# Kernel optimization log

Hardware: AMD Instinct MI355X
Metric: run time of the kernel (lower is better)

The kernel has to match this reference:

```python
import jax, jax.numpy as jnp
import numpy as np
from math import sqrt

N_IN = 1024
N_OUT = 1024
DEPTH = 10
N_NODES = 2 ** (DEPTH + 1) - 1  # 2047
BATCH = 32768


def setup_inputs() -> dict:
    key = jax.random.key(0)
    k1, k2, k3 = jax.random.split(key, 3)
    f1 = 1.0 / sqrt(N_IN)
    f2 = 1.0 / sqrt(DEPTH + 1)
    x = jax.random.normal(k1, (BATCH, N_IN), dtype=jnp.float32)
    w1s = jax.random.uniform(k2, (N_NODES, N_IN), dtype=jnp.float32, minval=-f1, maxval=f1)
    w2s = jax.random.uniform(k3, (N_NODES, N_OUT), dtype=jnp.float32, minval=-f2, maxval=f2)
    return {"x": x, "w1s": w1s, "w2s": w2s, "depth": DEPTH}


def reference(x, w1s, w2s, depth):
    batch = x.shape[0]

    def step(current_node, _):
        # current_node: [b] int32 node index at this tree level
        plane_score = jnp.einsum('bi,bi->b', x, w1s[current_node])  # [b]
        plane_choice = (plane_score > 0).astype(jnp.int32)
        next_node = current_node * 2 + plane_choice + 1
        return next_node, (current_node, plane_score)

    node0 = jnp.zeros((batch,), dtype=jnp.int32)
    _, (all_nodes, all_scores) = jax.lax.scan(step, node0, None, length=depth + 1)
    all_nodes = all_nodes.T    # [b, depth+1]
    all_scores = all_scores.T  # [b, depth+1]

    selected_w2s = w2s[all_nodes]  # [b, depth+1, nOut]
    y = jnp.einsum('bij,bi->bj', selected_w2s, all_scores)
    return y
```

## Files before the change

kernel.cpp:

```cpp
#include <hip/hip_runtime.h>


typedef float        f32x4 __attribute__((ext_vector_type(4)));
typedef unsigned int u32x4 __attribute__((ext_vector_type(4)));

#define FFF_BATCH  32768
#define FFF_NIN    1024
#define FFF_NOUT   1024
#define FFF_LEVELS 11
#define FFF_NODES  2047
#define FFF_EPS    0.035f

__device__ __forceinline__ f32x4 ld_nt4f(const f32x4* p) { return __builtin_nontemporal_load(p); }
__device__ __forceinline__ float ub(unsigned d, int k) {
    return (float)((d >> (8 * k)) & 0xffu);
}

__device__ __forceinline__ int sdot4(unsigned a, unsigned b, int c) {
#if __has_builtin(__builtin_amdgcn_sdot4)
    return __builtin_amdgcn_sdot4((int)a, (int)b, c, false);
#else
#pragma unroll
    for (int k = 0; k < 4; ++k) {
        const int ai = (int)(a << (24 - 8 * k)) >> 24;
        const int bi = (int)(b << (24 - 8 * k)) >> 24;
        c += ai * bi;
    }
    return c;
#endif
}

template<int CTRL>
__device__ __forceinline__ float dpp_add(float v) {
    const int t = __builtin_amdgcn_update_dpp(0, __float_as_int(v), CTRL, 0xF, 0xF, true);
    return v + __int_as_float(t);
}
__device__ __forceinline__ float wave_sum(float v) {
    v = dpp_add<0x111>(v); v = dpp_add<0x112>(v);
    v = dpp_add<0x114>(v); v = dpp_add<0x118>(v);
    v = dpp_add<0x142>(v); v = dpp_add<0x143>(v);
    return __int_as_float(__builtin_amdgcn_readlane(__float_as_int(v), 63));
}
template<int CTRL>
__device__ __forceinline__ int dpp_addi(int v) {
    return v + __builtin_amdgcn_update_dpp(0, v, CTRL, 0xF, 0xF, true);
}
__device__ __forceinline__ int wave_sum_i(int v) {
    v = dpp_addi<0x111>(v); v = dpp_addi<0x112>(v);
    v = dpp_addi<0x114>(v); v = dpp_addi<0x118>(v);
    v = dpp_addi<0x142>(v); v = dpp_addi<0x143>(v);
    return __builtin_amdgcn_readlane(v, 63);
}
template<int CTRL>
__device__ __forceinline__ float dpp_max(float v) {
    const int t = __builtin_amdgcn_update_dpp(0, __float_as_int(v), CTRL, 0xF, 0xF, true);
    return fmaxf(v, __int_as_float(t));
}
__device__ __forceinline__ float wave_max(float v) {
    v = dpp_max<0x111>(v); v = dpp_max<0x112>(v);
    v = dpp_max<0x114>(v); v = dpp_max<0x118>(v);
    v = dpp_max<0x142>(v); v = dpp_max<0x143>(v);
    return __int_as_float(__builtin_amdgcn_readlane(__float_as_int(v), 63));
}

__global__ void fff_quant_u8(const float* __restrict__ w1, const float* __restrict__ w2,
                             unsigned char* __restrict__ q1, unsigned char* __restrict__ q2,
                             float* __restrict__ s1, float* __restrict__ s2)
{
    const int node = blockIdx.x;
    const int t    = threadIdx.x;
    const int wave = t >> 6;
    const int lane = t & 63;

    const f32x4* r1 = reinterpret_cast<const f32x4*>(w1 + (size_t)node * FFF_NIN);
    const f32x4* r2 = reinterpret_cast<const f32x4*>(w2 + (size_t)node * FFF_NOUT);
    const int si = 64 * (t & 3) + (t >> 2);
    const f32x4 v1 = r1[si];
    const f32x4 v2 = r2[si];

    float m1 = 0.f, m2 = 0.f;
#pragma unroll
    for (int k = 0; k < 4; ++k) {
        m1 = fmaxf(m1, fabsf(v1[k]));
        m2 = fmaxf(m2, fabsf(v2[k]));
    }
#pragma unroll
    for (int m = 1; m < 64; m <<= 1) {
        m1 = fmaxf(m1, __shfl_xor(m1, m, 64));
        m2 = fmaxf(m2, __shfl_xor(m2, m, 64));
    }
    __shared__ float sm1[4], sm2[4];
    if (lane == 0) { sm1[wave] = m1; sm2[wave] = m2; }
    __syncthreads();
    m1 = fmaxf(fmaxf(sm1[0], sm1[1]), fmaxf(sm1[2], sm1[3]));
    m2 = fmaxf(fmaxf(sm2[0], sm2[1]), fmaxf(sm2[2], sm2[3]));

    const float st1 = (m1 > 0.f) ? m1 / 127.f : 1.f;
    const float st2 = (m2 > 0.f) ? m2 / 127.f : 1.f;
    if (t == 0) { s1[node] = st1; s2[node] = st2; }

    unsigned d1 = 0, d2 = 0;
#pragma unroll
    for (int k = 0; k < 4; ++k) {
        const int i1 = (int)rintf(v1[k] / st1);
        const int u2 = (int)rintf(v2[k] / st2) + 128;
        d1 |= ((unsigned)i1 & 0xffu) << (8 * k);
        d2 |= ((unsigned)u2 & 0xffu) << (8 * k);
    }
    reinterpret_cast<unsigned*>(q1)[(size_t)node * 256 + t] = d1;
    reinterpret_cast<unsigned*>(q2)[(size_t)node * 256 + t] = d2;
}

__global__ __launch_bounds__(256, 4) void fff_main_u8(
    const float*         __restrict__ x,
    const unsigned char* __restrict__ q1,
    const float*         __restrict__ s1,
    const float*         __restrict__ w1f,
    const unsigned char* __restrict__ q2,
    const float*         __restrict__ s2,
    float*               __restrict__ y)
{
    const int row  = blockIdx.x * 4 + (threadIdx.x >> 6);
    const int lane = threadIdx.x & 63;

    const f32x4* x4 = reinterpret_cast<const f32x4*>(x + (size_t)row * FFF_NIN);
    f32x4 xv[4];
#pragma unroll
    for (int c = 0; c < 4; ++c) xv[c] = ld_nt4f(&x4[c * 64 + lane]);

    float mx = 0.f;
#pragma unroll
    for (int c = 0; c < 4; ++c)
#pragma unroll
        for (int k = 0; k < 4; ++k) mx = fmaxf(mx, fabsf(xv[c][k]));
    mx = wave_max(mx);
    const float stx = (mx > 0.f) ? mx / 127.f : 1.f;
    const float inv = (mx > 0.f) ? 127.f / mx : 0.f;

    unsigned xq[4];
#pragma unroll
    for (int c = 0; c < 4; ++c) {
        const int a0 = (int)rintf(xv[c][0] * inv);
        const int a1 = (int)rintf(xv[c][1] * inv);
        const int a2 = (int)rintf(xv[c][2] * inv);
        const int a3 = (int)rintf(xv[c][3] * inv);
        xq[c] = ((unsigned)a0 & 0xffu) | (((unsigned)a1 & 0xffu) << 8) |
                (((unsigned)a2 & 0xffu) << 16) | (((unsigned)a3 & 0xffu) << 24);
    }

    f32x4 acc[4];
#pragma unroll
    for (int c = 0; c < 4; ++c) acc[c] = (f32x4)(0.f);
    float corr = 0.f;

    const u32x4* q1v = reinterpret_cast<const u32x4*>(q1);
    const u32x4* q2v = reinterpret_cast<const u32x4*>(q2);

    int node = 0;
    u32x4 d1 = q1v[lane];
    u32x4 d2 = q2v[lane];
    float sc1 = s1[0];
    float sc2 = s2[0];

#pragma unroll 1
    for (int l = 0; l < FFF_LEVELS; ++l) {
        int idot = 0;
#pragma unroll
        for (int c = 0; c < 4; ++c) idot = sdot4(xq[c], d1[c], idot);

        float p = (float)wave_sum_i(idot) * (stx * sc1);

        if (__builtin_expect(fabsf(p) < FFF_EPS, 0)) {
            const f32x4* w14 = reinterpret_cast<const f32x4*>(w1f + (size_t)node * FFF_NIN);
            float s = 0.f;
#pragma unroll
            for (int c = 0; c < 4; ++c) {
                const f32x4 w = w14[c * 64 + lane];
                s = fmaf(xv[c][0], w[0], s);
                s = fmaf(xv[c][1], w[1], s);
                s = fmaf(xv[c][2], w[2], s);
                s = fmaf(xv[c][3], w[3], s);
            }
            p = wave_sum(s);
        }

        const int next = 2 * node + 1 + ((p > 0.f) ? 1 : 0);
        u32x4 nd1 = d1, nd2 = d2;
        float ns1 = sc1, ns2 = sc2;
        if (l < FFF_LEVELS - 1) {
            const int un = __builtin_amdgcn_readfirstlane(next);
            nd1 = q1v[(size_t)un * 64 + lane];
            nd2 = q2v[(size_t)un * 64 + lane];
            ns1 = s1[un];
            ns2 = s2[un];
        }

        const float s2l = p * sc2;
        corr = fmaf(s2l, 128.f, corr);
#pragma unroll
        for (int c = 0; c < 4; ++c) {
#pragma unroll
            for (int k = 0; k < 4; ++k)
                acc[c][k] = fmaf(s2l, ub(d2[c], k), acc[c][k]);
        }

        node = next;
        d1 = nd1; d2 = nd2; sc1 = ns1; sc2 = ns2;
    }

    f32x4* y4 = reinterpret_cast<f32x4*>(y + (size_t)row * FFF_NOUT);
#pragma unroll
    for (int c = 0; c < 4; ++c) {
        f32x4 o;
        o[0] = acc[c][0] - corr; o[1] = acc[c][1] - corr;
        o[2] = acc[c][2] - corr; o[3] = acc[c][3] - corr;
        y4[c * 64 + lane] = o;
    }
}

__global__ __launch_bounds__(256, 4) void fff_fused_f32(
    const float* __restrict__ x, const float* __restrict__ w1s,
    const float* __restrict__ w2s, float* __restrict__ y)
{
    const int row  = blockIdx.x * 4 + (threadIdx.x >> 6);
    const int lane = threadIdx.x & 63;
    const f32x4* x4 = reinterpret_cast<const f32x4*>(x + (size_t)row * FFF_NIN);
    f32x4 xv[4];
#pragma unroll
    for (int c = 0; c < 4; ++c) xv[c] = x4[c * 64 + lane];
    f32x4 acc[4];
#pragma unroll
    for (int c = 0; c < 4; ++c) acc[c] = (f32x4)(0.f);
    int node = 0;
#pragma unroll 1
    for (int l = 0; l < FFF_LEVELS; ++l) {
        const f32x4* w14 = reinterpret_cast<const f32x4*>(w1s + (size_t)node * FFF_NIN);
        const f32x4* w24 = reinterpret_cast<const f32x4*>(w2s + (size_t)node * FFF_NOUT);
        f32x4 wv[4], uv[4];
#pragma unroll
        for (int c = 0; c < 4; ++c) { wv[c] = w14[c * 64 + lane]; uv[c] = w24[c * 64 + lane]; }
        float p = 0.f;
#pragma unroll
        for (int c = 0; c < 4; ++c) {
            p = fmaf(xv[c][0], wv[c][0], p); p = fmaf(xv[c][1], wv[c][1], p);
            p = fmaf(xv[c][2], wv[c][2], p); p = fmaf(xv[c][3], wv[c][3], p);
        }
#pragma unroll
        for (int m = 1; m < 64; m <<= 1) p += __shfl_xor(p, m, 64);
#pragma unroll
        for (int c = 0; c < 4; ++c) {
            acc[c][0] = fmaf(p, uv[c][0], acc[c][0]); acc[c][1] = fmaf(p, uv[c][1], acc[c][1]);
            acc[c][2] = fmaf(p, uv[c][2], acc[c][2]); acc[c][3] = fmaf(p, uv[c][3], acc[c][3]);
        }
        node = node * 2 + 1 + ((p > 0.f) ? 1 : 0);
    }
    f32x4* y4 = reinterpret_cast<f32x4*>(y + (size_t)row * FFF_NOUT);
#pragma unroll
    for (int c = 0; c < 4; ++c) y4[c * 64 + lane] = acc[c];
}

extern "C" void kernel_launch(void* const* d_in, const int* in_sizes, int n_in,
                              void* d_out, int out_size, void* d_ws, size_t ws_size,
                              hipStream_t stream) {
    const float* x   = (const float*)d_in[0];
    const float* w1s = (const float*)d_in[1];
    const float* w2s = (const float*)d_in[2];
    float* y = (float*)d_out;

    const size_t sc_bytes = 8192;
    const size_t q_bytes  = (size_t)FFF_NODES * 1024;
    const size_t need = 2 * sc_bytes + 2 * q_bytes;

    if (ws_size >= need) {
        float* s1 = (float*)d_ws;
        float* s2 = (float*)((char*)d_ws + sc_bytes);
        unsigned char* q1 = (unsigned char*)d_ws + 2 * sc_bytes;
        unsigned char* q2 = q1 + q_bytes;
        fff_quant_u8<<<FFF_NODES, 256, 0, stream>>>(w1s, w2s, q1, q2, s1, s2);
        fff_main_u8<<<FFF_BATCH / 4, 256, 0, stream>>>(x, q1, s1, w1s, q2, s2, y);
    } else {
        fff_fused_f32<<<FFF_BATCH / 4, 256, 0, stream>>>(x, w1s, w2s, y);
    }
}
```

Measured before the change: 80.45 us.

## Process two batch rows per wavefront with interleaved tree traversal

Each wavefront now handles two batch rows, interleaving their int8 dot products, paired DPP reductions and next-node weight loads, so the two independent dependency chains can hide each other's latency. The fp32 row data is no longer kept in registers; the rare exact-recheck path reloads x from memory instead. The grid is halved to match. This raises register pressure and may lower occupancy, and both rows' fallback branches can diverge in cost.

```diff
diff --git a/kernel.cpp b/kernel.cpp
--- a/kernel.cpp
+++ b/kernel.cpp
@@ -45,11 +45,15 @@
 __device__ __forceinline__ int dpp_addi(int v) {
     return v + __builtin_amdgcn_update_dpp(0, v, CTRL, 0xF, 0xF, true);
 }
-__device__ __forceinline__ int wave_sum_i(int v) {
-    v = dpp_addi<0x111>(v); v = dpp_addi<0x112>(v);
-    v = dpp_addi<0x114>(v); v = dpp_addi<0x118>(v);
-    v = dpp_addi<0x142>(v); v = dpp_addi<0x143>(v);
-    return __builtin_amdgcn_readlane(v, 63);
+__device__ __forceinline__ void wave_sum_i2(int& a, int& b) {
+    a = dpp_addi<0x111>(a); b = dpp_addi<0x111>(b);
+    a = dpp_addi<0x112>(a); b = dpp_addi<0x112>(b);
+    a = dpp_addi<0x114>(a); b = dpp_addi<0x114>(b);
+    a = dpp_addi<0x118>(a); b = dpp_addi<0x118>(b);
+    a = dpp_addi<0x142>(a); b = dpp_addi<0x142>(b);
+    a = dpp_addi<0x143>(a); b = dpp_addi<0x143>(b);
+    a = __builtin_amdgcn_readlane(a, 63);
+    b = __builtin_amdgcn_readlane(b, 63);
 }
 template<int CTRL>
 __device__ __forceinline__ float dpp_max(float v) {
@@ -120,101 +124,145 @@
     const float*         __restrict__ s2,
     float*               __restrict__ y)
 {
-    const int row  = blockIdx.x * 4 + (threadIdx.x >> 6);
+    const int wave = threadIdx.x >> 6;
     const int lane = threadIdx.x & 63;
-
-    const f32x4* x4 = reinterpret_cast<const f32x4*>(x + (size_t)row * FFF_NIN);
-    f32x4 xv[4];
-#pragma unroll
-    for (int c = 0; c < 4; ++c) xv[c] = ld_nt4f(&x4[c * 64 + lane]);
-
-    float mx = 0.f;
-#pragma unroll
-    for (int c = 0; c < 4; ++c)
-#pragma unroll
-        for (int k = 0; k < 4; ++k) mx = fmaxf(mx, fabsf(xv[c][k]));
-    mx = wave_max(mx);
-    const float stx = (mx > 0.f) ? mx / 127.f : 1.f;
-    const float inv = (mx > 0.f) ? 127.f / mx : 0.f;
-
-    unsigned xq[4];
-#pragma unroll
-    for (int c = 0; c < 4; ++c) {
-        const int a0 = (int)rintf(xv[c][0] * inv);
-        const int a1 = (int)rintf(xv[c][1] * inv);
-        const int a2 = (int)rintf(xv[c][2] * inv);
-        const int a3 = (int)rintf(xv[c][3] * inv);
-        xq[c] = ((unsigned)a0 & 0xffu) | (((unsigned)a1 & 0xffu) << 8) |
-                (((unsigned)a2 & 0xffu) << 16) | (((unsigned)a3 & 0xffu) << 24);
-    }
-
-    f32x4 acc[4];
-#pragma unroll
-    for (int c = 0; c < 4; ++c) acc[c] = (f32x4)(0.f);
-    float corr = 0.f;
+    const int row0 = (blockIdx.x * 4 + wave) * 2;
+
+    const f32x4* x4a = reinterpret_cast<const f32x4*>(x + (size_t)row0 * FFF_NIN);
+    const f32x4* x4b = reinterpret_cast<const f32x4*>(x + (size_t)(row0 + 1) * FFF_NIN);
+
+    unsigned xqa[4], xqb[4];
+    float stxa, stxb;
+    {
+        f32x4 xa[4], xb[4];
+#pragma unroll
+        for (int c = 0; c < 4; ++c) {
+            xa[c] = ld_nt4f(&x4a[c * 64 + lane]);
+            xb[c] = ld_nt4f(&x4b[c * 64 + lane]);
+        }
+        float ma = 0.f, mb = 0.f;
+#pragma unroll
+        for (int c = 0; c < 4; ++c)
+#pragma unroll
+            for (int k = 0; k < 4; ++k) {
+                ma = fmaxf(ma, fabsf(xa[c][k]));
+                mb = fmaxf(mb, fabsf(xb[c][k]));
+            }
+        ma = wave_max(ma); mb = wave_max(mb);
+        stxa = (ma > 0.f) ? ma / 127.f : 1.f;
+        stxb = (mb > 0.f) ? mb / 127.f : 1.f;
+        const float ia = (ma > 0.f) ? 127.f / ma : 0.f;
+        const float ib = (mb > 0.f) ? 127.f / mb : 0.f;
+#pragma unroll
+        for (int c = 0; c < 4; ++c) {
+            unsigned pa = 0, pb = 0;
+#pragma unroll
+            for (int k = 0; k < 4; ++k) {
+                pa |= ((unsigned)(int)rintf(xa[c][k] * ia) & 0xffu) << (8 * k);
+                pb |= ((unsigned)(int)rintf(xb[c][k] * ib) & 0xffu) << (8 * k);
+            }
+            xqa[c] = pa; xqb[c] = pb;
+        }
+    }
+
+    f32x4 accA[4], accB[4];
+#pragma unroll
+    for (int c = 0; c < 4; ++c) { accA[c] = (f32x4)(0.f); accB[c] = (f32x4)(0.f); }
+    float corrA = 0.f, corrB = 0.f;
 
     const u32x4* q1v = reinterpret_cast<const u32x4*>(q1);
     const u32x4* q2v = reinterpret_cast<const u32x4*>(q2);
 
-    int node = 0;
-    u32x4 d1 = q1v[lane];
-    u32x4 d2 = q2v[lane];
-    float sc1 = s1[0];
-    float sc2 = s2[0];
+    int nodeA = 0, nodeB = 0;
+    u32x4 d1a = q1v[lane];
+    u32x4 d2a = q2v[lane];
+    u32x4 d1b = d1a, d2b = d2a;
+    float s1a = s1[0], s2a = s2[0];
+    float s1b = s1a, s2b = s2a;
 
 #pragma unroll 1
     for (int l = 0; l < FFF_LEVELS; ++l) {
-        int idot = 0;
-#pragma unroll
-        for (int c = 0; c < 4; ++c) idot = sdot4(xq[c], d1[c], idot);
-
-        float p = (float)wave_sum_i(idot) * (stx * sc1);
-
-        if (__builtin_expect(fabsf(p) < FFF_EPS, 0)) {
-            const f32x4* w14 = reinterpret_cast<const f32x4*>(w1f + (size_t)node * FFF_NIN);
+        int ia = 0, ib = 0;
+#pragma unroll
+        for (int c = 0; c < 4; ++c) {
+            ia = sdot4(xqa[c], d1a[c], ia);
+            ib = sdot4(xqb[c], d1b[c], ib);
+        }
+        wave_sum_i2(ia, ib);
+        float pA = (float)ia * (stxa * s1a);
+        float pB = (float)ib * (stxb * s1b);
+
+        if (__builtin_expect(fabsf(pA) < FFF_EPS, 0)) {
+            const f32x4* w14 = reinterpret_cast<const f32x4*>(w1f + (size_t)nodeA * FFF_NIN);
             float s = 0.f;
 #pragma unroll
             for (int c = 0; c < 4; ++c) {
-                const f32x4 w = w14[c * 64 + lane];
-                s = fmaf(xv[c][0], w[0], s);
-                s = fmaf(xv[c][1], w[1], s);
-                s = fmaf(xv[c][2], w[2], s);
-                s = fmaf(xv[c][3], w[3], s);
-            }
-            p = wave_sum(s);
-        }
-
-        const int next = 2 * node + 1 + ((p > 0.f) ? 1 : 0);
-        u32x4 nd1 = d1, nd2 = d2;
-        float ns1 = sc1, ns2 = sc2;
+                const f32x4 xc = ld_nt4f(&x4a[c * 64 + lane]);
+                const f32x4 w  = w14[c * 64 + lane];
+                s = fmaf(xc[0], w[0], s);
+                s = fmaf(xc[1], w[1], s);
+                s = fmaf(xc[2], w[2], s);
+                s = fmaf(xc[3], w[3], s);
+            }
+            pA = wave_sum(s);
+        }
+        if (__builtin_expect(fabsf(pB) < FFF_EPS, 0)) {
+            const f32x4* w14 = reinterpret_cast<const f32x4*>(w1f + (size_t)nodeB * FFF_NIN);
+            float s = 0.f;
+#pragma unroll
+            for (int c = 0; c < 4; ++c) {
+                const f32x4 xc = ld_nt4f(&x4b[c * 64 + lane]);
+                const f32x4 w  = w14[c * 64 + lane];
+                s = fmaf(xc[0], w[0], s);
+                s = fmaf(xc[1], w[1], s);
+                s = fmaf(xc[2], w[2], s);
+                s = fmaf(xc[3], w[3], s);
+            }
+            pB = wave_sum(s);
+        }
+
+        const int nextA = 2 * nodeA + 1 + ((pA > 0.f) ? 1 : 0);
+        const int nextB = 2 * nodeB + 1 + ((pB > 0.f) ? 1 : 0);
+        u32x4 nd1a = d1a, nd2a = d2a, nd1b = d1b, nd2b = d2b;
+        float ns1a = s1a, ns2a = s2a, ns1b = s1b, ns2b = s2b;
         if (l < FFF_LEVELS - 1) {
-            const int un = __builtin_amdgcn_readfirstlane(next);
-            nd1 = q1v[(size_t)un * 64 + lane];
-            nd2 = q2v[(size_t)un * 64 + lane];
-            ns1 = s1[un];
-            ns2 = s2[un];
-        }
-
-        const float s2l = p * sc2;
-        corr = fmaf(s2l, 128.f, corr);
-#pragma unroll
-        for (int c = 0; c < 4; ++c) {
-#pragma unroll
-            for (int k = 0; k < 4; ++k)
-                acc[c][k] = fmaf(s2l, ub(d2[c], k), acc[c][k]);
-        }
-
-        node = next;
-        d1 = nd1; d2 = nd2; sc1 = ns1; sc2 = ns2;
-    }
-
-    f32x4* y4 = reinterpret_cast<f32x4*>(y + (size_t)row * FFF_NOUT);
+            const int ua = __builtin_amdgcn_readfirstlane(nextA);
+            const int ub_ = __builtin_amdgcn_readfirstlane(nextB);
+            nd1a = q1v[(size_t)ua * 64 + lane];
+            nd2a = q2v[(size_t)ua * 64 + lane];
+            nd1b = q1v[(size_t)ub_ * 64 + lane];
+            nd2b = q2v[(size_t)ub_ * 64 + lane];
+            ns1a = s1[ua]; ns2a = s2[ua];
+            ns1b = s1[ub_]; ns2b = s2[ub_];
+        }
+
+        const float fA = pA * s2a;
+        const float fB = pB * s2b;
+        corrA = fmaf(fA, 128.f, corrA);
+        corrB = fmaf(fB, 128.f, corrB);
+#pragma unroll
+        for (int c = 0; c < 4; ++c) {
+#pragma unroll
+            for (int k = 0; k < 4; ++k) {
+                accA[c][k] = fmaf(fA, ub(d2a[c], k), accA[c][k]);
+                accB[c][k] = fmaf(fB, ub(d2b[c], k), accB[c][k]);
+            }
+        }
+
+        nodeA = nextA; nodeB = nextB;
+        d1a = nd1a; d2a = nd2a; d1b = nd1b; d2b = nd2b;
+        s1a = ns1a; s2a = ns2a; s1b = ns1b; s2b = ns2b;
+    }
+
+    f32x4* y4a = reinterpret_cast<f32x4*>(y + (size_t)row0 * FFF_NOUT);
+    f32x4* y4b = reinterpret_cast<f32x4*>(y + (size_t)(row0 + 1) * FFF_NOUT);
 #pragma unroll
     for (int c = 0; c < 4; ++c) {
-        f32x4 o;
-        o[0] = acc[c][0] - corr; o[1] = acc[c][1] - corr;
-        o[2] = acc[c][2] - corr; o[3] = acc[c][3] - corr;
-        y4[c * 64 + lane] = o;
+        f32x4 oa, ob;
+#pragma unroll
+        for (int k = 0; k < 4; ++k) { oa[k] = accA[c][k] - corrA; ob[k] = accB[c][k] - corrB; }
+        y4a[c * 64 + lane] = oa;
+        y4b[c * 64 + lane] = ob;
     }
 }
 
@@ -277,7 +325,7 @@
         unsigned char* q1 = (unsigned char*)d_ws + 2 * sc_bytes;
         unsigned char* q2 = q1 + q_bytes;
         fff_quant_u8<<<FFF_NODES, 256, 0, stream>>>(w1s, w2s, q1, q2, s1, s2);
-        fff_main_u8<<<FFF_BATCH / 4, 256, 0, stream>>>(x, q1, s1, w1s, q2, s2, y);
+        fff_main_u8<<<FFF_BATCH / 8, 256, 0, stream>>>(x, q1, s1, w1s, q2, s2, y);
     } else {
         fff_fused_f32<<<FFF_BATCH / 4, 256, 0, stream>>>(x, w1s, w2s, y);
     }
```

Result: slower. 103.6 us (+28.8%).
